# Kernel tuning notes

Hardware: AMD Instinct MI355X
Metric: run time of the kernel (lower is better)

Reference implementation:

```python
import jax, jax.numpy as jnp
import numpy as np

H = 32      # query heads
HK = 8      # kv heads
HD = 64     # head dim
D = 2048    # model dim
BASE = 10000.0
NEG = -1e9


def _rope_cos_sin(L):
    inv_freq = 1.0 / (BASE ** (jnp.arange(0, HD, 2, dtype=jnp.float32) / HD))  # [HD/2]
    freqs = jnp.arange(L, dtype=jnp.float32)[:, None] * inv_freq[None, :]       # [L, HD/2]
    emb = jnp.concatenate([freqs, freqs], axis=-1)                               # [L, HD]
    return jnp.cos(emb), jnp.sin(emb)


def _rotate_half(x):
    x1, x2 = jnp.split(x, 2, axis=-1)
    return jnp.concatenate([-x2, x1], axis=-1)


def setup_inputs() -> dict:
    key = jax.random.key(0)
    ks = jax.random.split(key, 5)
    B, L = 2, 2048
    x = jax.random.normal(ks[0], (B, L, D), dtype=jnp.float32)
    Wq = jax.random.normal(ks[1], (D, D), dtype=jnp.float32) * 0.02
    Wk = jax.random.normal(ks[2], (HK * HD, D), dtype=jnp.float32) * 0.02
    Wv = jax.random.normal(ks[3], (HK * HD, D), dtype=jnp.float32) * 0.02
    Wo = jax.random.normal(ks[4], (D, D), dtype=jnp.float32) * 0.02
    causal = jnp.where(jnp.tril(jnp.ones((L, L), dtype=bool)), 0.0, NEG)
    mask = causal[None, None].astype(jnp.float32)  # [1,1,L,L] additive mask
    return {"x": x, "Wq": Wq, "Wk": Wk, "Wv": Wv, "Wo": Wo, "mask": mask}


def reference(x, Wq, Wk, Wv, Wo, mask):
    B, L, _ = x.shape
    # projections (nn.Linear: y = x @ W^T), split heads -> [B, heads, L, HD]
    q = jnp.einsum('bld,ed->ble', x, Wq).reshape(B, L, H, HD).transpose(0, 2, 1, 3)
    k = jnp.einsum('bld,ed->ble', x, Wk).reshape(B, L, HK, HD).transpose(0, 2, 1, 3)
    v = jnp.einsum('bld,ed->ble', x, Wv).reshape(B, L, HK, HD).transpose(0, 2, 1, 3)
    # RoPE (plain branch: L <= original_max); cos/sin [L,HD] broadcast over B,heads
    cos, sin = _rope_cos_sin(L)
    q = q * cos + _rotate_half(q) * sin
    k = k * cos + _rotate_half(k) * sin
    # GQA: repeat_interleave kv heads to H heads
    rep = H // HK
    k = jnp.repeat(k, rep, axis=1)  # [B,H,L,HD]
    v = jnp.repeat(v, rep, axis=1)
    scores = jnp.einsum('bhld,bhmd->bhlm', q, k) / np.float32(np.sqrt(HD)) + mask
    attn = jax.nn.softmax(scores, axis=-1)
    out = jnp.einsum('bhlm,bhmd->blhd', attn, v).reshape(B, L, D)
    return jnp.einsum('ble,de->bld', out, Wo)
```

## Files before the change

kernel.cpp:

```cpp
#include <hip/hip_runtime.h>
#include <math.h>

#define NH 32
#define NHK 8
#define HD 64
#define DMODEL 2048
#define LSEQ 2048
#define NB 2
#define QKV_N 3072

typedef __attribute__((ext_vector_type(8))) short short8;
typedef __attribute__((ext_vector_type(4))) float floatx4;

__device__ __forceinline__ unsigned short f2bf(float f) {
  unsigned u = __float_as_uint(f);
  return (unsigned short)((u + 0x7FFFu + ((u >> 16) & 1u)) >> 16);
}
__device__ __forceinline__ float bf2f(unsigned short v) {
  return __uint_as_float((unsigned)v << 16);
}
__device__ __forceinline__ float fast_exp2(float x) {
#if __has_builtin(__builtin_amdgcn_exp2f)
  return __builtin_amdgcn_exp2f(x);
#else
  return __expf(x * 0.69314718f);
#endif
}
__device__ __forceinline__ unsigned pack_bf_trunc(float hi, float lo) {
  return __builtin_amdgcn_perm(__float_as_uint(hi), __float_as_uint(lo), 0x07060302u);
}
__device__ __forceinline__ void stage16g(const char* g_lane,
                                         unsigned short* lds_wave_base, int lane) {
#if __has_builtin(__builtin_amdgcn_global_load_lds)
  __builtin_amdgcn_global_load_lds(
      (const __attribute__((address_space(1))) void*)(g_lane),
      (__attribute__((address_space(3))) void*)(lds_wave_base), 16, 0, 0);
#else
  *(uint4*)(lds_wave_base + lane * 8) = *(const uint4*)g_lane;
#endif
}

__global__ __launch_bounds__(256) void rope_tab(float2* __restrict__ tab) {
  int i = blockIdx.x * 256 + threadIdx.x;
  int d = i & 31, l = i >> 5;
  float invf = (float)pow(10000.0, -(double)d / 32.0);
  float ang = (float)l * invf;
  double sd, cd;
  sincos((double)ang, &sd, &cd);
  tab[i] = make_float2((float)cd, (float)sd);
}

__global__ __launch_bounds__(256) void cvt_bf16(const float* __restrict__ src,
                                                unsigned short* __restrict__ dst,
                                                int n4) {
  int i = blockIdx.x * 256 + threadIdx.x;
  if (i >= n4) return;
  float4 v = ((const float4*)src)[i];
  ushort4 o;
  o.x = f2bf(v.x); o.y = f2bf(v.y); o.z = f2bf(v.z); o.w = f2bf(v.w);
  ((ushort4*)dst)[i] = o;
}

__global__ __launch_bounds__(256) void cvt_w3(const float* __restrict__ Wq,
                                              const float* __restrict__ Wk,
                                              const float* __restrict__ Wv,
                                              unsigned short* __restrict__ dst) {
  const int NQ = DMODEL * DMODEL / 4, NK = 512 * DMODEL / 4;
  int i = blockIdx.x * 256 + threadIdx.x;
  const float* src;
  int off;
  if (i < NQ) { src = Wq; off = i; }
  else if (i < NQ + NK) { src = Wk; off = i - NQ; }
  else { src = Wv; off = i - NQ - NK; }
  float4 v = ((const float4*)src)[off];
  ushort4 o;
  o.x = f2bf(v.x); o.y = f2bf(v.y); o.z = f2bf(v.z); o.w = f2bf(v.w);
  ((ushort4*)dst)[i] = o;
}

template <int BN, bool BF16C>
__global__ __launch_bounds__(512, 2) void gemm8(const unsigned short* __restrict__ A,
                                                const unsigned short* __restrict__ B,
                                                void* __restrict__ Cv, int K, int ldc) {
  constexpr int CN = BN / 64;
  constexpr int BUFB = BN * 32;
  __shared__ unsigned short As[4 * 256 * 32];
  __shared__ unsigned short Bs[4 * BUFB];

  const int tid = threadIdx.x;
  const int wave = tid >> 6, lane = tid & 63;
  const int quad = lane >> 4, l16 = lane & 15;
  const int wm = wave & 1, wn = wave >> 1;

  const int nwg = gridDim.x * gridDim.y;
  const int orig = blockIdx.y * gridDim.x + blockIdx.x;
  const int swz = (orig & 7) * (nwg >> 3) + (orig >> 3);
  const int bx = swz % gridDim.x, by = swz / gridDim.x;
  const int m0 = by * 256, n0 = bx * BN;

  const int kt = K >> 5;

  const int sgrow = wave * 16 + (lane >> 2);
  const int cchunk = (lane & 3) ^ ((lane >> 3) & 3);
  const char* AgB = (const char*)(A + (size_t)(m0 + sgrow) * K + cchunk * 8);
  const char* BgB = (const char*)(B + (size_t)(n0 + sgrow) * K + cchunk * 8);

  auto stageA = [&](int t2) {
    unsigned short* dst = &As[((t2 & 3) << 13) + wave * 512];
#pragma unroll
    for (int u = 0; u < 2; ++u)
      stage16g(AgB + ((size_t)u * 128 * K + (size_t)t2 * 32) * 2, dst + u * 4096, lane);
  };
  auto stageB = [&](int t2) {
    unsigned short* dst = &Bs[(t2 & 3) * BUFB + wave * 512];
#pragma unroll
    for (int u = 0; u < BN / 128; ++u)
      stage16g(BgB + ((size_t)u * 128 * K + (size_t)t2 * 32) * 2, dst + u * 4096, lane);
  };

  const int sw8 = (quad ^ ((l16 >> 1) & 3)) * 8;

  floatx4 acc[8][CN] = {};

  stageA(0); stageB(0);
  stageA(1); stageB(1);
  stageA(2); stageB(2);

#pragma unroll 1
  for (int t = 0; t < kt; ++t) {
    if (t + 2 < kt) {
      if constexpr (BN == 256) asm volatile("s_waitcnt vmcnt(8)" ::: "memory");
      else                     asm volatile("s_waitcnt vmcnt(6)" ::: "memory");
    } else if (t + 1 < kt) {
      if constexpr (BN == 256) asm volatile("s_waitcnt vmcnt(4)" ::: "memory");
      else                     asm volatile("s_waitcnt vmcnt(3)" ::: "memory");
    } else {
      asm volatile("s_waitcnt vmcnt(0)" ::: "memory");
    }
    __builtin_amdgcn_s_barrier();
    __builtin_amdgcn_sched_barrier(0);

    const unsigned short* Asb = &As[(t & 3) << 13];
    const unsigned short* Bsb = &Bs[(t & 3) * BUFB];
    const unsigned short* Arow = Asb + (wm * 128 + l16) * 32 + sw8;
    const unsigned short* Brow = Bsb + (wn * 16 * CN + l16) * 32 + sw8;

    short8 bfr[CN], af[4];
#pragma unroll
    for (int j = 0; j < CN; ++j) bfr[j] = *(const short8*)(Brow + j * 16 * 32);
#pragma unroll
    for (int i = 0; i < 4; ++i) af[i] = *(const short8*)(Arow + i * 16 * 32);

    if (t + 3 < kt) stageA(t + 3);

    __builtin_amdgcn_s_setprio(1);
#pragma unroll
    for (int i = 0; i < 4; ++i)
#pragma unroll
      for (int j = 0; j < CN; ++j)
        acc[i][j] = __builtin_amdgcn_mfma_f32_16x16x32_bf16(af[i], bfr[j], acc[i][j], 0, 0, 0);
    __builtin_amdgcn_s_setprio(0);

#pragma unroll
    for (int i = 0; i < 4; ++i) af[i] = *(const short8*)(Arow + (64 + i * 16) * 32);

    if (t + 3 < kt) stageB(t + 3);

    __builtin_amdgcn_s_setprio(1);
#pragma unroll
    for (int i = 0; i < 4; ++i)
#pragma unroll
      for (int j = 0; j < CN; ++j)
        acc[4 + i][j] = __builtin_amdgcn_mfma_f32_16x16x32_bf16(af[i], bfr[j], acc[4 + i][j], 0, 0, 0);
    __builtin_amdgcn_s_setprio(0);
  }

#pragma unroll
  for (int i = 0; i < 8; ++i)
#pragma unroll
    for (int j = 0; j < CN; ++j)
#pragma unroll
      for (int r = 0; r < 4; ++r) {
        size_t idx = (size_t)(m0 + wm * 128 + i * 16 + quad * 4 + r) * ldc +
                     n0 + wn * 16 * CN + j * 16 + l16;
        if (BF16C)
          ((unsigned short*)Cv)[idx] = f2bf(acc[i][j][r]);
        else
          ((float*)Cv)[idx] = acc[i][j][r];
      }
}

__global__ __launch_bounds__(256) void ropek_cvt2(const unsigned short* __restrict__ qkvb,
                                                  const float2* __restrict__ tab,
                                                  unsigned short* __restrict__ kb) {
  int t = blockIdx.x * 256 + threadIdx.x;
  int d = t & 31;
  int rest = t >> 5;
  int khead = rest & 7;
  int bl = rest >> 3;
  int l = bl & (LSEQ - 1);
  int b = bl >> 11;
  const unsigned short* src = qkvb + (size_t)bl * QKV_N + DMODEL + khead * HD;
  float2 cs = tab[(size_t)l * 32 + d];
  float x1 = bf2f(src[d]), x2 = bf2f(src[d + 32]);
  unsigned short* dst = kb + ((size_t)((b * NHK + khead) * LSEQ + l)) * HD;
  dst[d] = f2bf(x1 * cs.x - x2 * cs.y);
  dst[d + 32] = f2bf(x2 * cs.x + x1 * cs.y);
}

__global__ __launch_bounds__(256) void vt_cvt2(const unsigned short* __restrict__ qkvb,
                                               unsigned short* __restrict__ vtb) {
  __shared__ unsigned short Lt[64][72];
  const int tt = blockIdx.x, kh = blockIdx.y, b = blockIdx.z;
  const int tid = threadIdx.x;
  const unsigned short* src =
      qkvb + ((size_t)(b * LSEQ + tt * 64)) * QKV_N + DMODEL + 512 + kh * HD;
  {
    int row = tid >> 2, c0 = (tid & 3) * 16;
    *(uint4*)&Lt[row][c0] = *(const uint4*)(src + (size_t)row * QKV_N + c0);
    *(uint4*)&Lt[row][c0 + 8] = *(const uint4*)(src + (size_t)row * QKV_N + c0 + 8);
  }
  __syncthreads();
  {
    int d = tid >> 2, seg = tid & 3;
    unsigned short o[16];
#pragma unroll
    for (int k = 0; k < 16; ++k) o[k] = Lt[seg * 16 + k][d];
    unsigned short* dst =
        vtb + ((size_t)((b * NHK + kh) * 80 + d)) * LSEQ + tt * 64 + seg * 16;
    *(uint4*)dst = *(uint4*)o;
    *(uint4*)(dst + 8) = *(uint4*)(o + 8);
  }
  if (tid < 64)
    vtb[((size_t)((b * NHK + kh) * 80 + 64)) * LSEQ + tt * 64 + tid] = 0x3F80;
}

__global__ __launch_bounds__(256, 2) void attn8(const unsigned short* __restrict__ qkvb,
                                                const float2* __restrict__ tab,
                                                const unsigned short* __restrict__ kb,
                                                const unsigned short* __restrict__ vtb,
                                                unsigned short* __restrict__ out) {
  const int kh = blockIdx.x;
  const int p = blockIdx.y;
  const int b = blockIdx.z;
  const int wave = threadIdx.x >> 6, lane = threadIdx.x & 63;
  const int quad = lane >> 4, l16 = lane & 15;
  const int h = kh * 4 + wave;

  __shared__ unsigned short Kbuf[2][64 * 64];
  __shared__ unsigned short Vbuf[2][80 * 64];
  __shared__ unsigned short Ps_all[4][32][72];
  unsigned short(*Ps)[72] = Ps_all[wave];

  const char* kbaseB = (const char*)(kb + ((size_t)(b * NHK + kh) * LSEQ) * HD);
  const char* vbaseB = (const char*)(vtb + ((size_t)(b * NHK + kh) * 80) * LSEQ);
  const float QSCALE = 0.125f * 1.44269504f;

  short8 qf[2][2];
  floatx4 O[2][5];

  auto loadQ = [&](int qb) {
#pragma unroll
    for (int i = 0; i < 2; ++i) {
      const int tok = qb + i * 16 + l16;
      const unsigned short* qr =
          qkvb + ((size_t)(b * LSEQ + tok)) * QKV_N + h * HD + quad * 8;
      uint4 lo = *(const uint4*)qr;
      uint4 hi = *(const uint4*)(qr + 32);
      const float2* tr = tab + (size_t)tok * 32 + quad * 8;
      float4 cs01 = ((const float4*)tr)[0];
      float4 cs23 = ((const float4*)tr)[1];
      float4 cs45 = ((const float4*)tr)[2];
      float4 cs67 = ((const float4*)tr)[3];
      float cosv[8] = {cs01.x, cs01.z, cs23.x, cs23.z, cs45.x, cs45.z, cs67.x, cs67.z};
      float sinv[8] = {cs01.y, cs01.w, cs23.y, cs23.w, cs45.y, cs45.w, cs67.y, cs67.w};
      const unsigned short* plo = (const unsigned short*)&lo;
      const unsigned short* phi = (const unsigned short*)&hi;
      unsigned short olo[8], ohi[8];
#pragma unroll
      for (int j = 0; j < 8; ++j) {
        float x1 = bf2f(plo[j]), x2 = bf2f(phi[j]);
        olo[j] = f2bf((x1 * cosv[j] - x2 * sinv[j]) * QSCALE);
        ohi[j] = f2bf((x2 * cosv[j] + x1 * sinv[j]) * QSCALE);
      }
      qf[i][0] = *(const short8*)olo;
      qf[i][1] = *(const short8*)ohi;
    }
  };
  auto zeroO = [&]() {
#pragma unroll
    for (int i = 0; i < 2; ++i)
#pragma unroll
      for (int j = 0; j < 5; ++j) O[i][j] = (floatx4){0.f, 0.f, 0.f, 0.f};
  };
  auto epilogue = [&](int qb) {
#pragma unroll
    for (int i = 0; i < 2; ++i) {
      float lv = __shfl(O[i][4][0], l16);
      float inv = 1.0f / lv;
      const size_t obase =
          ((size_t)(b * LSEQ + qb + i * 16 + l16)) * DMODEL + h * HD;
#pragma unroll
      for (int j = 0; j < 4; ++j) {
        uint2 w;
        w.x = (unsigned)f2bf(O[i][j][0] * inv) | ((unsigned)f2bf(O[i][j][1] * inv) << 16);
        w.y = (unsigned)f2bf(O[i][j][2] * inv) | ((unsigned)f2bf(O[i][j][3] * inv) << 16);
        *(uint2*)&out[obase + j * 16 + quad * 4] = w;
      }
    }
  };
  auto stageKV = [&](int bi, int kt) {
    unsigned short* Kd = Kbuf[bi];
    unsigned short* Vd = Vbuf[bi];
#pragma unroll
    for (int c = wave; c < 18; c += 4) {
      if (c < 8) {
        int o = c * 1024 + lane * 16;
        int row = o >> 7;
        int lgc = ((o >> 4) & 7) ^ (row & 7);
        stage16g(kbaseB + (size_t)(kt * 64 + row) * 128 + lgc * 16,
                 Kd + c * 512, lane);
      } else {
        int o = (c - 8) * 1024 + lane * 16;
        int row = o >> 7;
        int lgc = ((o >> 4) & 7) ^ (row & 7);
        stage16g(vbaseB + (size_t)row * (LSEQ * 2) + (size_t)kt * 128 + lgc * 16,
                 Vd + (c - 8) * 512, lane);
      }
    }
  };

  const int last0 = p >> 1;
  const int last1 = (63 - p) >> 1;
  const int qb0 = p * 32, qb1 = (63 - p) * 32;
  const int N = last0 + last1 + 2;

  loadQ(qb0);
  zeroO();
  stageKV(0, 0);
  int qb = qb0, lastk = last0;

#pragma unroll 1
  for (int m = 0; m < N; ++m) {
    __syncthreads();

    if (m + 1 < N) {
      int kt2 = (m + 1 > last0) ? (m - last0) : (m + 1);
      stageKV((m + 1) & 1, kt2);
    }
    if (m == last0 + 1) {
      epilogue(qb0);
      zeroO();
      loadQ(qb1);
      qb = qb1;
      lastk = last1;
    }

    const int kt = (m > last0) ? (m - last0 - 1) : m;
    const unsigned short* Ks = Kbuf[m & 1];
    const unsigned short* Vs = Vbuf[m & 1];

    short8 kf[4][2];
#pragma unroll
    for (int t = 0; t < 4; ++t)
#pragma unroll
      for (int hf = 0; hf < 2; ++hf) {
        int row = t * 16 + l16;
        int phys = (4 * hf + quad) ^ (row & 7);
        kf[t][hf] = *(const short8*)&Ks[row * 64 + phys * 8];
      }

    floatx4 st[4][2];
#pragma unroll
    for (int t = 0; t < 4; ++t)
#pragma unroll
      for (int i = 0; i < 2; ++i) {
        floatx4 z = {0.f, 0.f, 0.f, 0.f};
        z = __builtin_amdgcn_mfma_f32_16x16x32_bf16(kf[t][0], qf[i][0], z, 0, 0, 0);
        st[t][i] = __builtin_amdgcn_mfma_f32_16x16x32_bf16(kf[t][1], qf[i][1], z, 0, 0, 0);
      }

    if (kt == lastk) {
      const int kofs = kt * 64 - qb;
#pragma unroll
      for (int t = 0; t < 4; ++t) {
        const int krow = kofs + 16 * t + quad * 4;
#pragma unroll
        for (int i = 0; i < 2; ++i) {
          const int qcol = 16 * i + l16;
          float sv[4];
#pragma unroll
          for (int r = 0; r < 4; ++r) {
            float v = st[t][i][r];
            if (krow + r > qcol) v = -1e30f;
            sv[r] = fast_exp2(v);
          }
          uint2 w;
          w.x = pack_bf_trunc(sv[1], sv[0]);
          w.y = pack_bf_trunc(sv[3], sv[2]);
          *(uint2*)&Ps[16 * i + l16][16 * t + quad * 4] = w;
        }
      }
    } else {
#pragma unroll
      for (int t = 0; t < 4; ++t)
#pragma unroll
        for (int i = 0; i < 2; ++i) {
          float sv[4];
#pragma unroll
          for (int r = 0; r < 4; ++r) sv[r] = fast_exp2(st[t][i][r]);
          uint2 w;
          w.x = pack_bf_trunc(sv[1], sv[0]);
          w.y = pack_bf_trunc(sv[3], sv[2]);
          *(uint2*)&Ps[16 * i + l16][16 * t + quad * 4] = w;
        }
    }

    short8 pf[2][2];
#pragma unroll
    for (int i = 0; i < 2; ++i)
#pragma unroll
      for (int hh = 0; hh < 2; ++hh)
        pf[i][hh] = *(const short8*)&Ps[16 * i + l16][32 * hh + quad * 8];
#pragma unroll
    for (int j = 0; j < 5; ++j) {
      int row = j * 16 + l16;
      short8 vf0 = *(const short8*)&Vs[row * 64 + ((quad ^ (row & 7)) * 8)];
      short8 vf1 = *(const short8*)&Vs[row * 64 + (((4 + quad) ^ (row & 7)) * 8)];
#pragma unroll
      for (int i = 0; i < 2; ++i) {
        O[i][j] = __builtin_amdgcn_mfma_f32_16x16x32_bf16(vf0, pf[i][0], O[i][j], 0, 0, 0);
        O[i][j] = __builtin_amdgcn_mfma_f32_16x16x32_bf16(vf1, pf[i][1], O[i][j], 0, 0, 0);
      }
    }
  }

  epilogue(qb1);
}

extern "C" void kernel_launch(void* const* d_in, const int* in_sizes, int n_in,
                              void* d_out, int out_size, void* d_ws,
                              size_t ws_size, hipStream_t stream) {
  const float* x = (const float*)d_in[0];
  const float* Wq = (const float*)d_in[1];
  const float* Wk = (const float*)d_in[2];
  const float* Wv = (const float*)d_in[3];
  const float* Wo = (const float*)d_in[4];
  float* out = (float*)d_out;

  char* ws = (char*)d_ws;
  unsigned short* qkvb = (unsigned short*)ws;
  float2* tab = (float2*)(ws + 25165824);
  unsigned short* kbuf = (unsigned short*)(ws + 25690112);
  unsigned short* vtb = (unsigned short*)(ws + 29884416);
  unsigned short* xb = (unsigned short*)(ws + 35127296);
  unsigned short* wqkvb = (unsigned short*)(ws + 51904512);
  unsigned short* aob = xb;
  unsigned short* wob = wqkvb;

  const int M = NB * LSEQ;
  dim3 blk(256);

  rope_tab<<<(LSEQ * 32) / 256, blk, 0, stream>>>(tab);
  cvt_bf16<<<(M * DMODEL / 4 + 255) / 256, blk, 0, stream>>>(x, xb, M * DMODEL / 4);
  cvt_w3<<<(QKV_N * DMODEL / 4) / 256, blk, 0, stream>>>(Wq, Wk, Wv, wqkvb);

  gemm8<256, true><<<dim3(QKV_N / 256, M / 256), dim3(512), 0, stream>>>(
      xb, wqkvb, qkvb, DMODEL, QKV_N);

  ropek_cvt2<<<(NB * LSEQ * 8 * 32) / 256, blk, 0, stream>>>(qkvb, tab, kbuf);
  vt_cvt2<<<dim3(LSEQ / 64, NHK, NB), blk, 0, stream>>>(qkvb, vtb);

  attn8<<<dim3(NHK, 32, NB), blk, 0, stream>>>(qkvb, tab, kbuf, vtb, aob);

  cvt_bf16<<<(DMODEL * DMODEL / 4 + 255) / 256, blk, 0, stream>>>(Wo, wob, DMODEL * DMODEL / 4);

  gemm8<128, false><<<dim3(DMODEL / 128, M / 256), dim3(512), 0, stream>>>(
      aob, wob, out, DMODEL, DMODEL);
}
```

Baseline: 300.8 us.

## Split paired causal q-blocks into separate heavy-first workgroups and raise occupancy

The attention kernel no longer pairs a short and a long causal query block inside one workgroup. It launches one workgroup per 32-row query block, twice as many in total, ordered so the longest causal rows are scheduled first. The V staging buffer shrinks from 80 to 72 rows, since only the ones-row at index 64 is needed for the row-sum. Together with launch bounds raised to 3 blocks per SM, this is meant to fit more workgroups per CU and improve latency hiding and tail balance, at the cost of more per-block setup and less in-block work balancing.

Measured after the change: 303.6 us. No clear change (+0.9%).

```diff
diff --git a/kernel.cpp b/kernel.cpp
--- a/kernel.cpp
+++ b/kernel.cpp
@@ -235,20 +235,20 @@
     vtb[((size_t)((b * NHK + kh) * 80 + 64)) * LSEQ + tt * 64 + tid] = 0x3F80;
 }
 
-__global__ __launch_bounds__(256, 2) void attn8(const unsigned short* __restrict__ qkvb,
+__global__ __launch_bounds__(256, 3) void attn8(const unsigned short* __restrict__ qkvb,
                                                 const float2* __restrict__ tab,
                                                 const unsigned short* __restrict__ kb,
                                                 const unsigned short* __restrict__ vtb,
                                                 unsigned short* __restrict__ out) {
   const int kh = blockIdx.x;
-  const int p = blockIdx.y;
+  const int p = 63 - blockIdx.y;
   const int b = blockIdx.z;
   const int wave = threadIdx.x >> 6, lane = threadIdx.x & 63;
   const int quad = lane >> 4, l16 = lane & 15;
   const int h = kh * 4 + wave;
 
   __shared__ unsigned short Kbuf[2][64 * 64];
-  __shared__ unsigned short Vbuf[2][80 * 64];
+  __shared__ unsigned short Vbuf[2][72 * 64];
   __shared__ unsigned short Ps_all[4][32][72];
   unsigned short(*Ps)[72] = Ps_all[wave];
 
@@ -313,7 +313,7 @@
     unsigned short* Kd = Kbuf[bi];
     unsigned short* Vd = Vbuf[bi];
 #pragma unroll
-    for (int c = wave; c < 18; c += 4) {
+    for (int c = wave; c < 17; c += 4) {
       if (c < 8) {
         int o = c * 1024 + lane * 16;
         int row = o >> 7;
@@ -330,33 +330,21 @@
     }
   };
 
-  const int last0 = p >> 1;
-  const int last1 = (63 - p) >> 1;
-  const int qb0 = p * 32, qb1 = (63 - p) * 32;
-  const int N = last0 + last1 + 2;
-
-  loadQ(qb0);
+  const int qb = p * 32;
+  const int last = p >> 1;
+  const int N = last + 1;
+
+  loadQ(qb);
   zeroO();
   stageKV(0, 0);
-  int qb = qb0, lastk = last0;
 
 #pragma unroll 1
   for (int m = 0; m < N; ++m) {
     __syncthreads();
 
-    if (m + 1 < N) {
-      int kt2 = (m + 1 > last0) ? (m - last0) : (m + 1);
-      stageKV((m + 1) & 1, kt2);
-    }
-    if (m == last0 + 1) {
-      epilogue(qb0);
-      zeroO();
-      loadQ(qb1);
-      qb = qb1;
-      lastk = last1;
-    }
-
-    const int kt = (m > last0) ? (m - last0 - 1) : m;
+    if (m + 1 < N) stageKV((m + 1) & 1, m + 1);
+
+    const int kt = m;
     const unsigned short* Ks = Kbuf[m & 1];
     const unsigned short* Vs = Vbuf[m & 1];
 
@@ -380,7 +368,7 @@
         st[t][i] = __builtin_amdgcn_mfma_f32_16x16x32_bf16(kf[t][1], qf[i][1], z, 0, 0, 0);
       }
 
-    if (kt == lastk) {
+    if (kt == last) {
       const int kofs = kt * 64 - qb;
 #pragma unroll
       for (int t = 0; t < 4; ++t) {
@@ -424,7 +412,7 @@
         pf[i][hh] = *(const short8*)&Ps[16 * i + l16][32 * hh + quad * 8];
 #pragma unroll
     for (int j = 0; j < 5; ++j) {
-      int row = j * 16 + l16;
+      int row = (j == 4) ? (64 + (l16 & 7)) : (j * 16 + l16);
       short8 vf0 = *(const short8*)&Vs[row * 64 + ((quad ^ (row & 7)) * 8)];
       short8 vf1 = *(const short8*)&Vs[row * 64 + (((4 + quad) ^ (row & 7)) * 8)];
 #pragma unroll
@@ -435,7 +423,7 @@
     }
   }
 
-  epilogue(qb1);
+  epilogue(qb);
 }
 
 extern "C" void kernel_launch(void* const* d_in, const int* in_sizes, int n_in,
@@ -471,7 +459,7 @@
   ropek_cvt2<<<(NB * LSEQ * 8 * 32) / 256, blk, 0, stream>>>(qkvb, tab, kbuf);
   vt_cvt2<<<dim3(LSEQ / 64, NHK, NB), blk, 0, stream>>>(qkvb, vtb);
 
-  attn8<<<dim3(NHK, 32, NB), blk, 0, stream>>>(qkvb, tab, kbuf, vtb, aob);
+  attn8<<<dim3(NHK, 64, NB), blk, 0, stream>>>(qkvb, tab, kbuf, vtb, aob);
 
   cvt_bf16<<<(DMODEL * DMODEL / 4 + 255) / 256, blk, 0, stream>>>(Wo, wob, DMODEL * DMODEL / 4);
 
```
